# Performance work log

Hardware: AMD Instinct MI355X
Metric: run time of the kernel (lower is better)

Reference implementation:

```python
import jax, jax.numpy as jnp
import numpy as np

N_CLASSES = 1000
FEAT_DIM = 256
N = 65536


def setup_inputs() -> dict:
    key = jax.random.key(0)
    k1, k2, k3 = jax.random.split(key, 3)
    gt = jax.random.randint(k1, (N, N_CLASSES), 0, 2, dtype=jnp.int32)
    features = jax.random.normal(k2, (N, FEAT_DIM), dtype=jnp.float32)
    centers = jax.random.normal(k3, (N_CLASSES, FEAT_DIM), dtype=jnp.float32)
    return {"gt": gt, "features": features, "centers": centers}


def reference(gt, features, centers):
    # loss = (1/N) * sum_c sum_{i : gt[i,c] > 0} ||features[i] - centers[c]||^2
    # Vectorized via ||f||^2 + ||c||^2 - 2 f.c  (replaces the per-class python loop)
    mask = (gt > 0).astype(features.dtype)                      # [N, C]
    f_sq = jnp.sum(features * features, axis=1)                 # [N]
    c_sq = jnp.sum(centers * centers, axis=1)                   # [C]
    cross = features @ centers.T                                # [N, C]
    dist = f_sq[:, None] + c_sq[None, :] - 2.0 * cross          # [N, C]
    num_instances = features.shape[0]
    return jnp.sum(mask * dist) / num_instances
```

## Files before the change

kernel.cpp:

```cpp
#include <hip/hip_runtime.h>
#include <stdint.h>

#define N_ROWS 65536
#define N_CLS  1000
#define KPAD   1024
#define FEAT   256
#define MT     64
#define BK     64
#define NIT    (KPAD/BK)

typedef short bf16x8 __attribute__((ext_vector_type(8)));
typedef float f32x4  __attribute__((ext_vector_type(4)));

__device__ __forceinline__ ushort f32_to_bf16_rne(float f) {
    union { float f; uint32_t u; } x; x.f = f;
    uint32_t u = x.u + 0x7FFFu + ((x.u >> 16) & 1u);
    return (ushort)(u >> 16);
}

__global__ __launch_bounds__(256) void prep_kernel(const float* __restrict__ centers,
                                                   ushort* __restrict__ Bfrag,
                                                   float* __restrict__ csq,
                                                   float* __restrict__ out) {
    const int c = blockIdx.x;
    const int n = threadIdx.x;
    float v = 0.f;
    if (c < N_CLS) v = centers[(size_t)c * FEAT + n];

    const int it   = c >> 6;
    const int ks   = (c >> 5) & 1;
    const int quad = (c >> 3) & 3;
    const int j    = c & 7;
    const int w    = n >> 6;
    const int nt   = (n >> 4) & 3;
    const int ml   = n & 15;
    const int lane = quad * 16 + ml;
    const size_t idx = ((size_t)(((it * 2 + ks) * 4 + w) * 4 + nt) * 64 + lane) * 8 + j;
    Bfrag[idx] = f32_to_bf16_rne(v);

    float sq = v * v;
    #pragma unroll
    for (int off = 32; off > 0; off >>= 1) sq += __shfl_down(sq, off);
    __shared__ float red[4];
    if ((threadIdx.x & 63) == 0) red[threadIdx.x >> 6] = sq;
    __syncthreads();
    if (threadIdx.x == 0) {
        csq[c] = red[0] + red[1] + red[2] + red[3];
        if (c == 0) out[0] = 0.f;
    }
}

__global__ __launch_bounds__(256, 3) void main_kernel(const int* __restrict__ gt,
                                                      const float* __restrict__ features,
                                                      const ushort* __restrict__ Bfrag,
                                                      const float* __restrict__ csq,
                                                      float* __restrict__ out) {
    __shared__ ushort As[2 * 2 * 4 * 64 * 8];
    __shared__ float  csqS[KPAD];
    __shared__ float  rcS[256];
    __shared__ float  t2S[256];
    __shared__ float  rowcnt[MT];
    __shared__ float  t2row[MT];
    __shared__ float  blockred[4];

    const int tid  = threadIdx.x;
    const int m0   = blockIdx.x * MT;
    const int r    = tid >> 2;
    const int kc   = tid & 3;
    const int lane = tid & 63;
    const int w    = tid >> 6;
    const int ml   = lane & 15;
    const int quad = lane >> 4;

    f32x4 acc[4][4];
    #pragma unroll
    for (int i = 0; i < 4; i++)
        #pragma unroll
        for (int j = 0; j < 4; j++)
            #pragma unroll
            for (int k = 0; k < 4; k++) acc[i][j][k] = 0.f;

    int   rci = 0;
    float t2  = 0.f;
    const int* gtrow = gt + (size_t)(m0 + r) * N_CLS;

    const int mt_w = r >> 4, ml_w = r & 15;
    const int ks_w = kc >> 1, qb = (kc & 1) * 2;
    const int xw   = (ml_w >> 3) | (ks_w << 1) | ((kc & 1) << 2);
    const int slot0 = (((ks_w * 4 + mt_w) * 64) + (qb * 16 + ml_w)) ^ xw;
    const int slot1 = (((ks_w * 4 + mt_w) * 64) + ((qb + 1) * 16 + ml_w)) ^ xw;
    ushort* const wptr0 = As + slot0 * 8;
    ushort* const wptr1 = As + slot1 * 8;

    const int xr0 = ((lane >> 3) & 1) | (((lane >> 5) & 1) << 2);
    const int lx0 = (lane ^ xr0) * 8;
    const int lx1 = (lane ^ (xr0 | 2)) * 8;

    auto load_gt = [&](int it, int (&vv)[16]) {
        const int kb = it * BK + kc * 16;
        if (kb + 16 <= N_CLS) {
            const int4* p = (const int4*)(gtrow + kb);
            int4 a0 = p[0], a1 = p[1], a2 = p[2], a3 = p[3];
            vv[0]=a0.x;  vv[1]=a0.y;  vv[2]=a0.z;  vv[3]=a0.w;
            vv[4]=a1.x;  vv[5]=a1.y;  vv[6]=a1.z;  vv[7]=a1.w;
            vv[8]=a2.x;  vv[9]=a2.y;  vv[10]=a2.z; vv[11]=a2.w;
            vv[12]=a3.x; vv[13]=a3.y; vv[14]=a3.z; vv[15]=a3.w;
        } else {
            #pragma unroll
            for (int j = 0; j < 16; j++) {
                int k = kb + j;
                vv[j] = (k < N_CLS) ? gtrow[k] : 0;
            }
        }
    };

    auto convert_store = [&](int buf, int it, const int (&vv)[16]) {
        const int kb = it * BK + kc * 16;
        const float4* cp = (const float4*)&csqS[kb];
        float4 q0 = cp[0], q1 = cp[1], q2 = cp[2], q3 = cp[3];
        float cs[16] = {q0.x,q0.y,q0.z,q0.w, q1.x,q1.y,q1.z,q1.w,
                        q2.x,q2.y,q2.z,q2.w, q3.x,q3.y,q3.z,q3.w};
        uint32_t u[8];
        #pragma unroll
        for (int j = 0; j < 8; j++)
            u[j] = (uint32_t)(vv[2*j] + (vv[2*j+1] << 16)) * 0x3F80u;
        #pragma unroll
        for (int j = 0; j < 16; j++) {
            rci += vv[j];
            t2  += (float)vv[j] * cs[j];
        }
        uint4* d0 = (uint4*)(wptr0 + buf * 4096);
        uint4* d1 = (uint4*)(wptr1 + buf * 4096);
        *d0 = make_uint4(u[0], u[1], u[2], u[3]);
        *d1 = make_uint4(u[4], u[5], u[6], u[7]);
    };

    const ushort* bbase = Bfrag + ((size_t)w * 4) * 64 * 8 + (size_t)lane * 8;

    auto mfma_iter = [&](int buf, int it) {
        bf16x8 b0[4], b1[4];
        const ushort* p0 = bbase + (size_t)(it * 2 + 0) * (4 * 4 * 64 * 8);
        const ushort* p1 = bbase + (size_t)(it * 2 + 1) * (4 * 4 * 64 * 8);
        #pragma unroll
        for (int nt = 0; nt < 4; ++nt) b0[nt] = *(const bf16x8*)(p0 + nt * 64 * 8);
        #pragma unroll
        for (int nt = 0; nt < 4; ++nt) b1[nt] = *(const bf16x8*)(p1 + nt * 64 * 8);
        #pragma unroll
        for (int ks = 0; ks < 2; ++ks) {
            const int lx = ks ? lx1 : lx0;
            bf16x8 af[4];
            #pragma unroll
            for (int mt = 0; mt < 4; mt++)
                af[mt] = *(const bf16x8*)(As + buf * 4096 + (ks * 4 + mt) * 512 + lx);
            #pragma unroll
            for (int mt = 0; mt < 4; mt++)
                #pragma unroll
                for (int nt = 0; nt < 4; nt++)
                    acc[mt][nt] = __builtin_amdgcn_mfma_f32_16x16x32_bf16(
                        af[mt], ks ? b1[nt] : b0[nt], acc[mt][nt], 0, 0, 0);
        }
    };

    int gtA[16], gtB[16];
    {
        *(float4*)&csqS[tid * 4] = *(const float4*)&csq[tid * 4];
        load_gt(0, gtA);
        __syncthreads();
        convert_store(0, 0, gtA);
        load_gt(1, gtA);
        __syncthreads();
    }

    for (int it = 0; it < NIT; it += 2) {
        if (it + 2 < NIT) load_gt(it + 2, gtB);
        mfma_iter(0, it);
        if (it + 1 < NIT) convert_store(1, it + 1, gtA);
        __syncthreads();

        if (it + 3 < NIT) load_gt(it + 3, gtA);
        mfma_iter(1, it + 1);
        if (it + 2 < NIT) convert_store(0, it + 2, gtB);
        __syncthreads();
    }

    rcS[tid] = (float)rci;
    t2S[tid] = t2;
    __syncthreads();
    if (tid < MT) {
        rowcnt[tid] = rcS[tid*4] + rcS[tid*4+1] + rcS[tid*4+2] + rcS[tid*4+3];
        t2row[tid]  = t2S[tid*4] + t2S[tid*4+1] + t2S[tid*4+2] + t2S[tid*4+3];
    }
    __syncthreads();

    float part = 0.f;
    #pragma unroll
    for (int mt = 0; mt < 4; mt++) {
        #pragma unroll
        for (int nt = 0; nt < 4; nt++) {
            const int n = w * 64 + nt * 16 + ml;
            #pragma unroll
            for (int reg = 0; reg < 4; reg++) {
                const int ri = mt * 16 + quad * 4 + reg;
                const float f = features[(size_t)(m0 + ri) * FEAT + n];
                const float T = acc[mt][nt][reg];
                part += f * (rowcnt[ri] * f - 2.f * T) + t2row[ri] * (1.f / 256.f);
            }
        }
    }
    #pragma unroll
    for (int off = 32; off > 0; off >>= 1) part += __shfl_down(part, off);
    if (lane == 0) blockred[w] = part;
    __syncthreads();
    if (tid == 0)
        atomicAdd(out, (blockred[0] + blockred[1] + blockred[2] + blockred[3]) *
                           (1.f / (float)N_ROWS));
}

extern "C" void kernel_launch(void* const* d_in, const int* in_sizes, int n_in,
                              void* d_out, int out_size, void* d_ws, size_t ws_size,
                              hipStream_t stream) {
    const int*   gt       = (const int*)d_in[0];
    const float* features = (const float*)d_in[1];
    const float* centers  = (const float*)d_in[2];
    float*       out      = (float*)d_out;

    ushort* Bfrag = (ushort*)d_ws;
    float*  csq   = (float*)((char*)d_ws + (size_t)FEAT * KPAD * 2);

    prep_kernel<<<KPAD, 256, 0, stream>>>(centers, Bfrag, csq, out);
    main_kernel<<<N_ROWS / MT, 256, 0, stream>>>(gt, features, Bfrag, csq, out);
}
```

Baseline: 420.6 us.

## Split gt into a bit-packing pass and a bitmask-driven MFMA kernel

A streaming compress kernel first reads the int32 gt matrix once. It packs each row into a 1000-bit mask and computes per-row counts and the t2 sums. The GEMM kernel then rebuilds the bf16 A fragments from the bitmask held in LDS instead of converting gt in a software-pipelined loop, and drops the per-iteration syncthreads. This separates the bandwidth-bound gt read from the MFMA loop, at the cost of an extra launch and an 8 MB workspace round-trip; the old fused path remains as a fallback when the workspace is too small.

```diff
diff --git a/kernel.cpp b/kernel.cpp
--- a/kernel.cpp
+++ b/kernel.cpp
@@ -6,8 +6,8 @@
 #define KPAD   1024
 #define FEAT   256
 #define MT     64
-#define BK     64
-#define NIT    (KPAD/BK)
+#define NSTG   32
+#define NIT    16
 
 typedef short bf16x8 __attribute__((ext_vector_type(8)));
 typedef float f32x4  __attribute__((ext_vector_type(4)));
@@ -27,15 +27,14 @@
     float v = 0.f;
     if (c < N_CLS) v = centers[(size_t)c * FEAT + n];
 
-    const int it   = c >> 6;
-    const int ks   = (c >> 5) & 1;
+    const int s    = c >> 5;
     const int quad = (c >> 3) & 3;
     const int j    = c & 7;
     const int w    = n >> 6;
     const int nt   = (n >> 4) & 3;
     const int ml   = n & 15;
     const int lane = quad * 16 + ml;
-    const size_t idx = ((size_t)(((it * 2 + ks) * 4 + w) * 4 + nt) * 64 + lane) * 8 + j;
+    const size_t idx = (((size_t)(s * 4 + w) * 4 + nt) * 64 + lane) * 8 + j;
     Bfrag[idx] = f32_to_bf16_rne(v);
 
     float sq = v * v;
@@ -50,18 +49,171 @@
     }
 }
 
-__global__ __launch_bounds__(256, 3) void main_kernel(const int* __restrict__ gt,
-                                                      const float* __restrict__ features,
-                                                      const ushort* __restrict__ Bfrag,
-                                                      const float* __restrict__ csq,
-                                                      float* __restrict__ out) {
+
+__global__ __launch_bounds__(256) void compress_kernel(const int* __restrict__ gt,
+                                                       const float* __restrict__ csq,
+                                                       ushort* __restrict__ bitmask,
+                                                       float* __restrict__ rowcnt,
+                                                       float* __restrict__ t2row) {
+    __shared__ float csqS[KPAD];
+    const int tid  = threadIdx.x;
+    *(float4*)&csqS[tid * 4] = *(const float4*)&csq[tid * 4];
+    __syncthreads();
+    const int lane = tid & 63;
+    const int wid  = blockIdx.x * 4 + (tid >> 6);
+
+    float4 cs[4];
+    #pragma unroll
+    for (int j = 0; j < 4; j++) cs[j] = *(const float4*)&csqS[j * 256 + lane * 4];
+    const bool v3 = (768 + lane * 4) < N_CLS;
+
+    auto ldrow = [&](int row, int4 (&d)[4]) {
+        const int* g = gt + (size_t)row * N_CLS + lane * 4;
+        d[0] = *(const int4*)(g);
+        d[1] = *(const int4*)(g + 256);
+        d[2] = *(const int4*)(g + 512);
+        d[3] = v3 ? *(const int4*)(g + 768) : make_int4(0, 0, 0, 0);
+    };
+    auto proc = [&](int row, const int4 (&d)[4]) {
+        uint32_t p =
+              (uint32_t)d[0].x        | ((uint32_t)d[0].y << 1)  | ((uint32_t)d[0].z << 2)  | ((uint32_t)d[0].w << 3)
+            | ((uint32_t)d[1].x << 4) | ((uint32_t)d[1].y << 5)  | ((uint32_t)d[1].z << 6)  | ((uint32_t)d[1].w << 7)
+            | ((uint32_t)d[2].x << 8) | ((uint32_t)d[2].y << 9)  | ((uint32_t)d[2].z << 10) | ((uint32_t)d[2].w << 11)
+            | ((uint32_t)d[3].x << 12)| ((uint32_t)d[3].y << 13) | ((uint32_t)d[3].z << 14) | ((uint32_t)d[3].w << 15);
+        float t = (float)d[0].x * cs[0].x + (float)d[0].y * cs[0].y
+                + (float)d[0].z * cs[0].z + (float)d[0].w * cs[0].w
+                + (float)d[1].x * cs[1].x + (float)d[1].y * cs[1].y
+                + (float)d[1].z * cs[1].z + (float)d[1].w * cs[1].w
+                + (float)d[2].x * cs[2].x + (float)d[2].y * cs[2].y
+                + (float)d[2].z * cs[2].z + (float)d[2].w * cs[2].w
+                + (float)d[3].x * cs[3].x + (float)d[3].y * cs[3].y
+                + (float)d[3].z * cs[3].z + (float)d[3].w * cs[3].w;
+        int rc = __popc(p);
+        #pragma unroll
+        for (int off = 1; off < 64; off <<= 1) {
+            rc += __shfl_xor(rc, off);
+            t  += __shfl_xor(t, off);
+        }
+        bitmask[(size_t)row * 64 + lane] = (ushort)p;
+        if (lane == 0) { rowcnt[row] = (float)rc; t2row[row] = t; }
+    };
+
+    int4 dP[4], dQ[4];
+    ldrow(wid, dP);
+    ldrow(wid + 8192, dQ);
+    #pragma unroll
+    for (int rr = 0; rr < 8; rr += 2) {
+        if (rr + 2 < 8) { proc(wid + rr * 8192, dP); ldrow(wid + (rr + 2) * 8192, dP); }
+        else              proc(wid + rr * 8192, dP);
+        if (rr + 3 < 8) { proc(wid + (rr + 1) * 8192, dQ); ldrow(wid + (rr + 3) * 8192, dQ); }
+        else              proc(wid + (rr + 1) * 8192, dQ);
+    }
+}
+
+__global__ __launch_bounds__(256, 3) void main2_kernel(const ushort* __restrict__ bitmask,
+                                                       const float* __restrict__ features,
+                                                       const ushort* __restrict__ Bfrag,
+                                                       const float* __restrict__ rowcnt,
+                                                       const float* __restrict__ t2row,
+                                                       float* __restrict__ out) {
+    __shared__ uint32_t bmS[MT * 33];
+    __shared__ float    rcS[MT], t2S[MT], blockred[4];
+
+    const int tid  = threadIdx.x;
+    const int lane = tid & 63;
+    const int w    = tid >> 6;
+    const int ml   = lane & 15;
+    const int quad = lane >> 4;
+    const int m0   = blockIdx.x * MT;
+
+    const uint32_t* bm = (const uint32_t*)bitmask + (size_t)m0 * 32;
+    #pragma unroll
+    for (int i = 0; i < 8; i++) {
+        int idx = i * 256 + tid;
+        bmS[(idx >> 5) * 33 + (idx & 31)] = bm[idx];
+    }
+    if (tid < MT) rcS[tid] = rowcnt[m0 + tid];
+    else if (tid < 2 * MT) t2S[tid - MT] = t2row[m0 + tid - MT];
+    __syncthreads();
+
+    f32x4 acc[4][4];
+    #pragma unroll
+    for (int i = 0; i < 4; i++)
+        #pragma unroll
+        for (int j = 0; j < 4; j++)
+            #pragma unroll
+            for (int k = 0; k < 4; k++) acc[i][j][k] = 0.f;
+
+    const ushort* bb = Bfrag + ((size_t)w * 4 * 64 + lane) * 8;
+    auto ld_B = [&](int s, bf16x8 (&b)[4]) {
+        const ushort* p = bb + (size_t)s * 8192;
+        b[0] = *(const bf16x8*)(p);
+        b[1] = *(const bf16x8*)(p + 512);
+        b[2] = *(const bf16x8*)(p + 1024);
+        b[3] = *(const bf16x8*)(p + 1536);
+    };
+
+    auto dostage = [&](int s, const bf16x8 (&b)[4]) {
+        const int dw = (s & 7) * 4 + quad;
+        const int sb = (s >> 3) * 4;
+        #pragma unroll
+        for (int mt = 0; mt < 4; mt++) {
+            const uint32_t W = bmS[(mt * 16 + ml) * 33 + dw];
+            union { uint32_t u[4]; bf16x8 v; } a;
+            #pragma unroll
+            for (int p = 0; p < 4; p++) {
+                const int b0 = (p < 2) ? (sb + 2 * p) : (16 + sb + 2 * (p - 2));
+                a.u[p] = ((W >> b0) & 1u) * 0x3F80u
+                       | ((W >> (b0 + 1)) & 1u) * 0x3F800000u;
+            }
+            #pragma unroll
+            for (int nt = 0; nt < 4; nt++)
+                acc[mt][nt] = __builtin_amdgcn_mfma_f32_16x16x32_bf16(
+                    a.v, b[nt], acc[mt][nt], 0, 0, 0);
+        }
+    };
+
+    bf16x8 BfP[4], BfQ[4];
+    ld_B(0, BfP);
+    ld_B(1, BfQ);
+    for (int s = 0; s < NSTG; s += 2) {
+        dostage(s, BfP);
+        if (s + 2 < NSTG) ld_B(s + 2, BfP);
+        dostage(s + 1, BfQ);
+        if (s + 3 < NSTG) ld_B(s + 3, BfQ);
+    }
+
+    float part = 0.f;
+    #pragma unroll
+    for (int mt = 0; mt < 4; mt++) {
+        #pragma unroll
+        for (int nt = 0; nt < 4; nt++) {
+            const int n = w * 64 + nt * 16 + ml;
+            #pragma unroll
+            for (int reg = 0; reg < 4; reg++) {
+                const int ri = mt * 16 + quad * 4 + reg;
+                const float f = features[(size_t)(m0 + ri) * FEAT + n];
+                part += f * (rcS[ri] * f - 2.f * acc[mt][nt][reg]) + t2S[ri] * (1.f / 256.f);
+            }
+        }
+    }
+    #pragma unroll
+    for (int off = 32; off > 0; off >>= 1) part += __shfl_down(part, off);
+    if (lane == 0) blockred[w] = part;
+    __syncthreads();
+    if (tid == 0)
+        atomicAdd(out, (blockred[0] + blockred[1] + blockred[2] + blockred[3]) *
+                           (1.f / (float)N_ROWS));
+}
+
+__global__ __launch_bounds__(256, 3) void fused_kernel(const int* __restrict__ gt,
+                                                       const float* __restrict__ features,
+                                                       const ushort* __restrict__ Bfrag,
+                                                       const float* __restrict__ csq,
+                                                       float* __restrict__ out) {
     __shared__ ushort As[2 * 2 * 4 * 64 * 8];
     __shared__ float  csqS[KPAD];
-    __shared__ float  rcS[256];
-    __shared__ float  t2S[256];
-    __shared__ float  rowcnt[MT];
-    __shared__ float  t2row[MT];
-    __shared__ float  blockred[4];
+    __shared__ float  rcS[256], t2S[256], rowcnt[MT], t2row[MT], blockred[4];
 
     const int tid  = threadIdx.x;
     const int m0   = blockIdx.x * MT;
@@ -97,7 +249,7 @@
     const int lx1 = (lane ^ (xr0 | 2)) * 8;
 
     auto load_gt = [&](int it, int (&vv)[16]) {
-        const int kb = it * BK + kc * 16;
+        const int kb = it * 64 + kc * 16;
         if (kb + 16 <= N_CLS) {
             const int4* p = (const int4*)(gtrow + kb);
             int4 a0 = p[0], a1 = p[1], a2 = p[2], a3 = p[3];
@@ -115,7 +267,7 @@
     };
 
     auto convert_store = [&](int buf, int it, const int (&vv)[16]) {
-        const int kb = it * BK + kc * 16;
+        const int kb = it * 64 + kc * 16;
         const float4* cp = (const float4*)&csqS[kb];
         float4 q0 = cp[0], q1 = cp[1], q2 = cp[2], q3 = cp[3];
         float cs[16] = {q0.x,q0.y,q0.z,q0.w, q1.x,q1.y,q1.z,q1.w,
@@ -125,10 +277,7 @@
         for (int j = 0; j < 8; j++)
             u[j] = (uint32_t)(vv[2*j] + (vv[2*j+1] << 16)) * 0x3F80u;
         #pragma unroll
-        for (int j = 0; j < 16; j++) {
-            rci += vv[j];
-            t2  += (float)vv[j] * cs[j];
-        }
+        for (int j = 0; j < 16; j++) { rci += vv[j]; t2 += (float)vv[j] * cs[j]; }
         uint4* d0 = (uint4*)(wptr0 + buf * 4096);
         uint4* d1 = (uint4*)(wptr1 + buf * 4096);
         *d0 = make_uint4(u[0], u[1], u[2], u[3]);
@@ -136,7 +285,6 @@
     };
 
     const ushort* bbase = Bfrag + ((size_t)w * 4) * 64 * 8 + (size_t)lane * 8;
-
     auto mfma_iter = [&](int buf, int it) {
         bf16x8 b0[4], b1[4];
         const ushort* p0 = bbase + (size_t)(it * 2 + 0) * (4 * 4 * 64 * 8);
@@ -170,13 +318,11 @@
         load_gt(1, gtA);
         __syncthreads();
     }
-
     for (int it = 0; it < NIT; it += 2) {
         if (it + 2 < NIT) load_gt(it + 2, gtB);
         mfma_iter(0, it);
         if (it + 1 < NIT) convert_store(1, it + 1, gtA);
         __syncthreads();
-
         if (it + 3 < NIT) load_gt(it + 3, gtA);
         mfma_iter(1, it + 1);
         if (it + 2 < NIT) convert_store(0, it + 2, gtB);
@@ -202,8 +348,7 @@
             for (int reg = 0; reg < 4; reg++) {
                 const int ri = mt * 16 + quad * 4 + reg;
                 const float f = features[(size_t)(m0 + ri) * FEAT + n];
-                const float T = acc[mt][nt][reg];
-                part += f * (rowcnt[ri] * f - 2.f * T) + t2row[ri] * (1.f / 256.f);
+                part += f * (rowcnt[ri] * f - 2.f * acc[mt][nt][reg]) + t2row[ri] * (1.f / 256.f);
             }
         }
     }
@@ -224,9 +369,21 @@
     const float* centers  = (const float*)d_in[2];
     float*       out      = (float*)d_out;
 
-    ushort* Bfrag = (ushort*)d_ws;
-    float*  csq   = (float*)((char*)d_ws + (size_t)FEAT * KPAD * 2);
+    char* ws = (char*)d_ws;
+    ushort* Bfrag = (ushort*)(ws);
+    float*  csq   = (float*)(ws + 524288);
 
     prep_kernel<<<KPAD, 256, 0, stream>>>(centers, Bfrag, csq, out);
-    main_kernel<<<N_ROWS / MT, 256, 0, stream>>>(gt, features, Bfrag, csq, out);
-}
+
+    const size_t REQ = 524288u + 4096u + 262144u + 262144u + 8388608u;
+    if (ws_size >= REQ) {
+        float*  rowcnt  = (float*)(ws + 528384);
+        float*  t2row   = (float*)(ws + 790528);
+        ushort* bitmask = (ushort*)(ws + 1052672);
+        compress_kernel<<<2048, 256, 0, stream>>>(gt, csq, bitmask, rowcnt, t2row);
+        main2_kernel<<<N_ROWS / MT, 256, 0, stream>>>(bitmask, features, Bfrag,
+                                                      rowcnt, t2row, out);
+    } else {
+        fused_kernel<<<N_ROWS / MT, 256, 0, stream>>>(gt, features, Bfrag, csq, out);
+    }
+}
```

Result: slower. 432.7 us (+2.9%).
